# Kernel tuning notes

Measured on AMD Instinct MI355X. Metric: run time of the kernel, lower is better.

## Reference

```python
import jax, jax.numpy as jnp
import numpy as np

GRID_H, GRID_W, INPUT_DIM = 256, 256, 64
BATCH = 4096


def setup_inputs() -> dict:
    key = jax.random.key(0)
    k_in, k_w = jax.random.split(key)
    inputs = jax.random.uniform(k_in, (BATCH, INPUT_DIM), dtype=jnp.float32)
    # SOM weights initialized uniform[0,1) as in the original layer
    weights_map = jax.random.uniform(k_w, (GRID_H, GRID_W, INPUT_DIM), dtype=jnp.float32)
    return {"inputs": inputs, "weights_map": weights_map}


def reference(inputs, weights_map):
    """Inference forward of SOM2dLayer: find BMU coords + quantization error.

    inputs:      [B, D]
    weights_map: [H, W, D]
    returns (bmu_indices [B,2] int32, quantization_errors [B] float32)
    """
    H, W, D = weights_map.shape
    flat_w = weights_map.reshape(H * W, D)            # [N, D]
    x2 = jnp.sum(inputs * inputs, axis=1, keepdims=True)      # [B, 1]
    w2 = jnp.sum(flat_w * flat_w, axis=1)                     # [N]
    d2 = x2 - 2.0 * (inputs @ flat_w.T) + w2                  # [B, N]
    d2 = jnp.maximum(d2, 0.0)                                 # numerical floor
    bmu_flat = jnp.argmin(d2, axis=1)                         # [B]
    bmu_y = (bmu_flat // W).astype(jnp.int32)
    bmu_x = (bmu_flat % W).astype(jnp.int32)
    bmu_indices = jnp.stack([bmu_y, bmu_x], axis=1)           # [B, 2]
    min_d2 = jnp.take_along_axis(d2, bmu_flat[:, None], axis=1)[:, 0]
    quantization_errors = jnp.sqrt(min_d2)                    # [B]
    return bmu_indices, quantization_errors
```

## Files before the change

kernel.cpp:

```cpp
#include <hip/hip_runtime.h>
#include <math.h>


typedef short  bf16x8 __attribute__((ext_vector_type(8)));
typedef float  f32x4  __attribute__((ext_vector_type(4)));
typedef unsigned short u16;

constexpr int D     = 64;
constexpr int NW    = 65536;
constexpr int B     = 4096;
constexpr int NSUB  = 256;
constexpr int NFINE = NW / 16;
constexpr float MARG_HALF = 0.15f;

constexpr int NRANGE = 128;
constexpr int RBKB   = 8;

__device__ inline u16 bf16u(float f) {
    union { float f; unsigned u; } v; v.f = f;
    unsigned b = v.u;
    b += 0x7fffu + ((b >> 16) & 1u);
    return (u16)(b >> 16);
}

__device__ inline u16 bf16up(float f) {
    union { float f; unsigned u; } v; v.f = f;
    unsigned h = v.u >> 16;
    if ((v.u & 0xFFFFu) && !(v.u >> 31)) h += 1;
    return (u16)h;
}

__global__ __launch_bounds__(256) void k_prep(const float* __restrict__ w,
                                              const float* __restrict__ x,
                                              u16* __restrict__ whi,
                                              u16* __restrict__ xhi,
                                              float* __restrict__ w2c) {
    const int idx = blockIdx.x * 256 + threadIdx.x;
    if (idx < NW) {
        const float4* wr = reinterpret_cast<const float4*>(w + (size_t)idx * D);
        u16* orow = whi + (size_t)idx * D;
        float a0 = 0.f, a1 = 0.f, a2 = 0.f, a3 = 0.f;
#pragma unroll
        for (int h = 0; h < 8; ++h) {
            float4 v0 = wr[2 * h], v1 = wr[2 * h + 1];
            a0 = fmaf(v0.x, v0.x, a0); a1 = fmaf(v0.y, v0.y, a1);
            a2 = fmaf(v0.z, v0.z, a2); a3 = fmaf(v0.w, v0.w, a3);
            a0 = fmaf(v1.x, v1.x, a0); a1 = fmaf(v1.y, v1.y, a1);
            a2 = fmaf(v1.z, v1.z, a2); a3 = fmaf(v1.w, v1.w, a3);
            bf16x8 o = {(short)bf16u(v0.x), (short)bf16u(v0.y),
                        (short)bf16u(v0.z), (short)bf16u(v0.w),
                        (short)bf16u(v1.x), (short)bf16u(v1.y),
                        (short)bf16u(v1.z), (short)bf16u(v1.w)};
            *reinterpret_cast<bf16x8*>(orow + 8 * h) = o;
        }
        w2c[idx] = -0.5f * ((a0 + a1) + (a2 + a3));
    } else {
        const int r = idx - NW;
        const float4* xr = reinterpret_cast<const float4*>(x + (size_t)r * D);
        u16* orow = xhi + (size_t)r * D;
#pragma unroll
        for (int h = 0; h < 8; ++h) {
            float4 v0 = xr[2 * h], v1 = xr[2 * h + 1];
            bf16x8 o = {(short)bf16u(v0.x), (short)bf16u(v0.y),
                        (short)bf16u(v0.z), (short)bf16u(v0.w),
                        (short)bf16u(v1.x), (short)bf16u(v1.y),
                        (short)bf16u(v1.z), (short)bf16u(v1.w)};
            *reinterpret_cast<bf16x8*>(orow + 8 * h) = o;
        }
    }
}

template <int WRITE_FINE>
__global__ __launch_bounds__(256, 2) void k_screen0(
        const u16* __restrict__ whi, const u16* __restrict__ xhi,
        const float* __restrict__ w2c, float* __restrict__ pmt,
        u16* __restrict__ pmf) {
    __shared__ __align__(16) u16 fsh[4][2048];
    const int bid  = blockIdx.x;
    const int nr   = bid & (NRANGE - 1);
    const int tid  = threadIdx.x;
    const int wv   = tid >> 6;
    const int lane = tid & 63;
    const int col  = lane & 15;
    const int kg   = lane >> 4;
    const int rbk  = (bid >> 7) * 4 + wv;
    const int row0 = rbk * 128;
    const int W0   = nr * 512;

    bf16x8 a[8][2];
#pragma unroll
    for (int rg = 0; rg < 8; ++rg)
#pragma unroll
        for (int h = 0; h < 2; ++h)
            a[rg][h] = *reinterpret_cast<const bf16x8*>(
                xhi + (size_t)(row0 + rg * 16 + col) * D + h * 32 + kg * 8);

    float mx[8][4];
#pragma unroll
    for (int rg = 0; rg < 8; ++rg)
#pragma unroll
        for (int r = 0; r < 4; ++r) mx[rg][r] = -3.4e38f;

    bf16x8 pb[3][4];
    float  pc[3][2];

    const u16* wl = whi + (size_t)(W0 + col) * D + kg * 8;

    for (int ch = 0; ch < 2; ++ch) {
        const int pbase = ch * 8;
#pragma unroll
        for (int s = 0; s < 2; ++s) {
            const int pp = pbase + s;
            const u16* p0 = wl + (size_t)pp * 32 * D;
            const u16* p1 = p0 + 16 * D;
            pb[s][0] = *reinterpret_cast<const bf16x8*>(p0);
            pb[s][1] = *reinterpret_cast<const bf16x8*>(p0 + 32);
            pb[s][2] = *reinterpret_cast<const bf16x8*>(p1);
            pb[s][3] = *reinterpret_cast<const bf16x8*>(p1 + 32);
            pc[s][0] = w2c[W0 + pp * 32 + col];
            pc[s][1] = w2c[W0 + pp * 32 + 16 + col];
        }

#pragma unroll
        for (int mp = 0; mp < 8; ++mp) {
            if (mp + 2 < 8) {
                constexpr int dummy = 0; (void)dummy;
                const int sl = (mp + 2) % 3;
                const int pp = pbase + mp + 2;
                const u16* p0 = wl + (size_t)pp * 32 * D;
                const u16* p1 = p0 + 16 * D;
                pb[sl][0] = *reinterpret_cast<const bf16x8*>(p0);
                pb[sl][1] = *reinterpret_cast<const bf16x8*>(p0 + 32);
                pb[sl][2] = *reinterpret_cast<const bf16x8*>(p1);
                pb[sl][3] = *reinterpret_cast<const bf16x8*>(p1 + 32);
                pc[sl][0] = w2c[W0 + pp * 32 + col];
                pc[sl][1] = w2c[W0 + pp * 32 + 16 + col];
            }
            __builtin_amdgcn_sched_barrier(0);

            const int cs = mp % 3;
            const f32x4 cq0 = {pc[cs][0], pc[cs][0], pc[cs][0], pc[cs][0]};
            const f32x4 cq1 = {pc[cs][1], pc[cs][1], pc[cs][1], pc[cs][1]};
#pragma unroll
            for (int rg = 0; rg < 8; ++rg) {
                f32x4 acc = __builtin_amdgcn_mfma_f32_16x16x32_bf16(a[rg][0], pb[cs][0], cq0, 0, 0, 0);
                acc = __builtin_amdgcn_mfma_f32_16x16x32_bf16(a[rg][1], pb[cs][1], acc, 0, 0, 0);
                mx[rg][0] = fmaxf(mx[rg][0], acc[0]);
                mx[rg][1] = fmaxf(mx[rg][1], acc[1]);
                mx[rg][2] = fmaxf(mx[rg][2], acc[2]);
                mx[rg][3] = fmaxf(mx[rg][3], acc[3]);
            }
#pragma unroll
            for (int rg = 0; rg < 8; ++rg) {
                f32x4 acc = __builtin_amdgcn_mfma_f32_16x16x32_bf16(a[rg][0], pb[cs][2], cq1, 0, 0, 0);
                acc = __builtin_amdgcn_mfma_f32_16x16x32_bf16(a[rg][1], pb[cs][3], acc, 0, 0, 0);
                mx[rg][0] = fmaxf(mx[rg][0], acc[0]);
                mx[rg][1] = fmaxf(mx[rg][1], acc[1]);
                mx[rg][2] = fmaxf(mx[rg][2], acc[2]);
                mx[rg][3] = fmaxf(mx[rg][3], acc[3]);
            }
        }

        const int sub = nr * 2 + ch;

        if (WRITE_FINE) {
#pragma unroll
            for (int rg = 0; rg < 8; ++rg)
#pragma unroll
                for (int r = 0; r < 4; ++r)
                    fsh[wv][(rg * 16 + kg * 4 + r) * 16 + col] = bf16up(mx[rg][r]);
        }

#pragma unroll
        for (int rg = 0; rg < 8; ++rg) {
            float v0 = mx[rg][0], v1 = mx[rg][1], v2 = mx[rg][2], v3 = mx[rg][3];
#pragma unroll
            for (int sh = 1; sh < 16; sh <<= 1) {
                v0 = fmaxf(v0, __shfl_xor(v0, sh, 64));
                v1 = fmaxf(v1, __shfl_xor(v1, sh, 64));
                v2 = fmaxf(v2, __shfl_xor(v2, sh, 64));
                v3 = fmaxf(v3, __shfl_xor(v3, sh, 64));
            }
            float vv = v0;
            vv = (col == 1) ? v1 : vv;
            vv = (col == 2) ? v2 : vv;
            vv = (col == 3) ? v3 : vv;
            if (col < 4)
                pmt[(size_t)sub * B + row0 + rg * 16 + kg * 4 + col] = vv;
            mx[rg][0] = -3.4e38f; mx[rg][1] = -3.4e38f;
            mx[rg][2] = -3.4e38f; mx[rg][3] = -3.4e38f;
        }

        if (WRITE_FINE) {
            const char* src = reinterpret_cast<const char*>(&fsh[wv][0]);
            char* dst = (char*)pmf + ((size_t)sub * 32 + rbk) * 4096;
#pragma unroll
            for (int i = 0; i < 4; ++i)
                *reinterpret_cast<float4*>(dst + i * 1024 + lane * 16) =
                    *reinterpret_cast<const float4*>(src + i * 1024 + lane * 16);
        }
    }
}

template <int FINE>
__global__ __launch_bounds__(256) void k_rescore(
        const float* __restrict__ x, const float* __restrict__ w,
        const float* __restrict__ w2c, const float* __restrict__ pmt,
        const u16* __restrict__ pmf, float* __restrict__ out) {
    const int wv   = threadIdx.x >> 6;
    const int lane = threadIdx.x & 63;
    const int row  = blockIdx.x * 4 + wv;
    const int rbk2 = row >> 7;
    const int rl   = row & 127;

    float pv[4];
#pragma unroll
    for (int it = 0; it < 4; ++it)
        pv[it] = pmt[(size_t)(it * 64 + lane) * B + row];
    float gm = fmaxf(fmaxf(pv[0], pv[1]), fmaxf(pv[2], pv[3]));
#pragma unroll
    for (int s = 1; s < 64; s <<= 1) gm = fmaxf(gm, __shfl_xor(gm, s, 64));
    const float thr = gm - MARG_HALF;

    const float4* xr = reinterpret_cast<const float4*>(x + (size_t)row * D);
    float4 xq[16];
#pragma unroll
    for (int q = 0; q < 16; ++q) xq[q] = xr[q];

    float bestv = 3.4e38f;
    int   besti = 0x7fffffff;

#pragma unroll
    for (int it = 0; it < 4; ++it) {
        unsigned long long bm = __ballot(pv[it] >= thr);
        while (bm) {
            int sb = __ffsll(bm) - 1;
            bm &= bm - 1;
            int sub  = it * 64 + sb;
            int base = sub * 256;

            if (FINE) {
                float fv = -3.4e38f;
                if (lane < 16) {
                    union { unsigned u; float f; } c;
                    c.u = (unsigned)pmf[((size_t)sub * 32 + rbk2) * 2048
                                        + rl * 16 + lane] << 16;
                    fv = c.f;
                }
                unsigned long long fm = __ballot(fv >= thr);
                while (fm) {
                    int colq = __ffsll(fm) - 1;
                    fm &= fm - 1;
                    int j = lane & 15, q = lane >> 4;
                    int n = base + j * 16 + colq;
                    const float4* wr = reinterpret_cast<const float4*>(w + (size_t)n * D);
                    float d0 = 0.f, d1 = 0.f, d2 = 0.f, d3 = 0.f;
#pragma unroll
                    for (int k = 0; k < 4; ++k) {
                        float4 wq = wr[q * 4 + k];
                        float4 xv = xq[q * 4 + k];
                        d0 = fmaf(xv.x, wq.x, d0); d1 = fmaf(xv.y, wq.y, d1);
                        d2 = fmaf(xv.z, wq.z, d2); d3 = fmaf(xv.w, wq.w, d3);
                    }
                    float d = (d0 + d1) + (d2 + d3);
                    d += __shfl_xor(d, 16, 64);
                    d += __shfl_xor(d, 32, 64);
                    float val = -2.f * (d + w2c[n]);
                    if (val < bestv || (val == bestv && n < besti)) { bestv = val; besti = n; }
                }
            } else {
#pragma unroll
                for (int p4 = 0; p4 < 4; ++p4) {
                    int n = base + p4 * 64 + lane;
                    const float4* wr = reinterpret_cast<const float4*>(w + (size_t)n * D);
                    float d0 = 0.f, d1 = 0.f, d2 = 0.f, d3 = 0.f;
#pragma unroll
                    for (int q = 0; q < 16; ++q) {
                        float4 wq = wr[q];
                        d0 = fmaf(xq[q].x, wq.x, d0);
                        d1 = fmaf(xq[q].y, wq.y, d1);
                        d2 = fmaf(xq[q].z, wq.z, d2);
                        d3 = fmaf(xq[q].w, wq.w, d3);
                    }
                    float dot = (d0 + d1) + (d2 + d3);
                    float val = -2.f * (dot + w2c[n]);
                    if (val < bestv || (val == bestv && n < besti)) { bestv = val; besti = n; }
                }
            }
        }
    }
#pragma unroll
    for (int s = 1; s < 64; s <<= 1) {
        float ov = __shfl_xor(bestv, s, 64);
        int   oi = __shfl_xor(besti, s, 64);
        if (ov < bestv || (ov == bestv && oi < besti)) { bestv = ov; besti = oi; }
    }
    if (lane == 0) {
        float a0 = 0.f, a1 = 0.f, a2 = 0.f, a3 = 0.f;
#pragma unroll
        for (int q = 0; q < 16; ++q) {
            a0 = fmaf(xq[q].x, xq[q].x, a0);
            a1 = fmaf(xq[q].y, xq[q].y, a1);
            a2 = fmaf(xq[q].z, xq[q].z, a2);
            a3 = fmaf(xq[q].w, xq[q].w, a3);
        }
        float x2 = (a0 + a1) + (a2 + a3);
        float d2f = x2 + bestv;
        if (d2f < 0.f) d2f = 0.f;
        out[row * 2 + 0] = (float)(besti >> 8);
        out[row * 2 + 1] = (float)(besti & 255);
        out[2 * B + row] = sqrtf(d2f);
    }
}

__global__ __launch_bounds__(256) void fb_w2(const float* __restrict__ w,
                                             float* __restrict__ w2) {
    int n = blockIdx.x * 256 + threadIdx.x;
    const float4* wr = reinterpret_cast<const float4*>(w + (size_t)n * D);
    float a0 = 0.f, a1 = 0.f, a2 = 0.f, a3 = 0.f;
#pragma unroll
    for (int q = 0; q < 16; ++q) {
        float4 v = wr[q];
        a0 = fmaf(v.x, v.x, a0); a1 = fmaf(v.y, v.y, a1);
        a2 = fmaf(v.z, v.z, a2); a3 = fmaf(v.w, v.w, a3);
    }
    w2[n] = (a0 + a1) + (a2 + a3);
}

__global__ __launch_bounds__(256) void fb_main(const float* __restrict__ x,
                                               const float* __restrict__ w,
                                               const float* __restrict__ w2,
                                               float* __restrict__ ps,
                                               int* __restrict__ pi) {
    constexpr int NSTRIP = NW / 32;
    const int rb    = blockIdx.x & 15;
    const int strip = blockIdx.x >> 4;
    const int row   = rb * 256 + threadIdx.x;
    float xr[D];
    const float4* xrow = reinterpret_cast<const float4*>(x + (size_t)row * D);
#pragma unroll
    for (int q = 0; q < 16; ++q) {
        float4 v = xrow[q];
        xr[q * 4 + 0] = v.x; xr[q * 4 + 1] = v.y;
        xr[q * 4 + 2] = v.z; xr[q * 4 + 3] = v.w;
    }
    float best = 3.4e38f; int bidx = 0;
    const int n0 = strip * NSTRIP, n1 = n0 + NSTRIP;
    for (int n = n0; n < n1; ++n) {
        const float* wr = w + (size_t)n * D;
        float a0 = 0.f, a1 = 0.f, a2 = 0.f, a3 = 0.f;
#pragma unroll
        for (int d = 0; d < D; d += 4) {
            a0 = fmaf(xr[d + 0], wr[d + 0], a0);
            a1 = fmaf(xr[d + 1], wr[d + 1], a1);
            a2 = fmaf(xr[d + 2], wr[d + 2], a2);
            a3 = fmaf(xr[d + 3], wr[d + 3], a3);
        }
        float s = fmaf(-2.f, (a0 + a1) + (a2 + a3), w2[n]);
        if (s < best) { best = s; bidx = n; }
    }
    ps[(size_t)strip * B + row] = best;
    pi[(size_t)strip * B + row] = bidx;
}

__global__ __launch_bounds__(256) void fb_merge(const float* __restrict__ x,
                                                const float* __restrict__ ps,
                                                const int* __restrict__ pi,
                                                float* __restrict__ out) {
    int row = blockIdx.x * 256 + threadIdx.x;
    float bs = 3.5e38f; int bi = 0;
    for (int t = 0; t < 32; ++t) {
        float s = ps[(size_t)t * B + row];
        int   i = pi[(size_t)t * B + row];
        if (s < bs || (s == bs && i < bi)) { bs = s; bi = i; }
    }
    const float4* xrow = reinterpret_cast<const float4*>(x + (size_t)row * D);
    float a0 = 0.f, a1 = 0.f, a2 = 0.f, a3 = 0.f;
#pragma unroll
    for (int q = 0; q < 16; ++q) {
        float4 v = xrow[q];
        a0 = fmaf(v.x, v.x, a0); a1 = fmaf(v.y, v.y, a1);
        a2 = fmaf(v.z, v.z, a2); a3 = fmaf(v.w, v.w, a3);
    }
    float x2 = (a0 + a1) + (a2 + a3);
    float d2 = x2 + bs;
    if (d2 < 0.f) d2 = 0.f;
    out[row * 2 + 0] = (float)(bi >> 8);
    out[row * 2 + 1] = (float)(bi & 255);
    out[2 * B + row] = sqrtf(d2);
}

extern "C" void kernel_launch(void* const* d_in, const int* in_sizes, int n_in,
                              void* d_out, int out_size, void* d_ws, size_t ws_size,
                              hipStream_t stream) {
    const float* x = (const float*)d_in[0];
    const float* w = (const float*)d_in[1];
    float* out = (float*)d_out;

    const size_t whi_sz = (size_t)NW * D * 2;
    const size_t xhi_sz = (size_t)B * D * 2;
    const size_t w2c_sz = (size_t)NW * 4;
    const size_t pm_sz  = (size_t)B * NSUB * 4;
    const size_t pmf_sz = (size_t)NFINE * B * 2;
    const size_t need_c = whi_sz + xhi_sz + w2c_sz + pm_sz;
    const size_t need_f = need_c + pmf_sz;

    if (ws_size >= need_c) {
        char* p = (char*)d_ws;
        u16*   whi = (u16*)p;   p += whi_sz;
        u16*   xhi = (u16*)p;   p += xhi_sz;
        float* w2c = (float*)p; p += w2c_sz;
        float* pmt = (float*)p; p += pm_sz;
        u16*   pmf = (u16*)p;

        k_prep<<<(NW + B) / 256, 256, 0, stream>>>(w, x, whi, xhi, w2c);
        if (ws_size >= need_f) {
            k_screen0<1><<<NRANGE * RBKB, 256, 0, stream>>>(whi, xhi, w2c, pmt, pmf);
            k_rescore<1><<<B / 4, 256, 0, stream>>>(x, w, w2c, pmt, pmf, out);
        } else {
            k_screen0<0><<<NRANGE * RBKB, 256, 0, stream>>>(whi, xhi, w2c, pmt, pmf);
            k_rescore<0><<<B / 4, 256, 0, stream>>>(x, w, w2c, pmt, pmf, out);
        }
    } else {
        float* w2 = (float*)d_ws;
        float* ps = w2 + NW;
        int*   pi = (int*)(ps + (size_t)32 * B);
        fb_w2<<<NW / 256, 256, 0, stream>>>(w, w2);
        fb_main<<<16 * 32, 256, 0, stream>>>(x, w, w2, ps, pi);
        fb_merge<<<B / 256, 256, 0, stream>>>(x, ps, pi, out);
    }
}
```

Before: 115.9 us.

## Split prep rows across four threads and store per-row maxima row-major

The prep kernel now has four threads handle each 64-element row, using shuffles to reduce the squared norm. This gives more parallelism and better-coalesced loads than one thread per row. The per-subrange maxima buffer changes from subrange-major to row-major: screen writes two adjacent floats per row, and rescore reads each row's 256 maxima contiguously. A sched_barrier in the screen loop is also removed, which leaves instruction scheduling to the compiler.

```diff
diff --git a/kernel.cpp b/kernel.cpp
--- a/kernel.cpp
+++ b/kernel.cpp
@@ -4,6 +4,7 @@
 
 typedef short  bf16x8 __attribute__((ext_vector_type(8)));
 typedef float  f32x4  __attribute__((ext_vector_type(4)));
+typedef float  f32x2  __attribute__((ext_vector_type(2)));
 typedef unsigned short u16;
 
 constexpr int D     = 64;
@@ -35,13 +36,16 @@
                                               u16* __restrict__ whi,
                                               u16* __restrict__ xhi,
                                               float* __restrict__ w2c) {
-    const int idx = blockIdx.x * 256 + threadIdx.x;
-    if (idx < NW) {
-        const float4* wr = reinterpret_cast<const float4*>(w + (size_t)idx * D);
-        u16* orow = whi + (size_t)idx * D;
+    const int t = blockIdx.x * 256 + threadIdx.x;
+    if (t < 4 * NW) {
+        const int row = t >> 2;
+        const int q4  = t & 3;
+        const float4* wr = reinterpret_cast<const float4*>(
+            w + (size_t)row * D + q4 * 16);
+        u16* orow = whi + (size_t)row * D + q4 * 16;
         float a0 = 0.f, a1 = 0.f, a2 = 0.f, a3 = 0.f;
 #pragma unroll
-        for (int h = 0; h < 8; ++h) {
+        for (int h = 0; h < 2; ++h) {
             float4 v0 = wr[2 * h], v1 = wr[2 * h + 1];
             a0 = fmaf(v0.x, v0.x, a0); a1 = fmaf(v0.y, v0.y, a1);
             a2 = fmaf(v0.z, v0.z, a2); a3 = fmaf(v0.w, v0.w, a3);
@@ -53,13 +57,19 @@
                         (short)bf16u(v1.z), (short)bf16u(v1.w)};
             *reinterpret_cast<bf16x8*>(orow + 8 * h) = o;
         }
-        w2c[idx] = -0.5f * ((a0 + a1) + (a2 + a3));
+        float p = (a0 + a1) + (a2 + a3);
+        p += __shfl_xor(p, 1, 64);
+        p += __shfl_xor(p, 2, 64);
+        if (q4 == 0) w2c[row] = -0.5f * p;
     } else {
-        const int r = idx - NW;
-        const float4* xr = reinterpret_cast<const float4*>(x + (size_t)r * D);
-        u16* orow = xhi + (size_t)r * D;
-#pragma unroll
-        for (int h = 0; h < 8; ++h) {
+        const int t2  = t - 4 * NW;
+        const int row = t2 >> 2;
+        const int q4  = t2 & 3;
+        const float4* xr = reinterpret_cast<const float4*>(
+            x + (size_t)row * D + q4 * 16);
+        u16* orow = xhi + (size_t)row * D + q4 * 16;
+#pragma unroll
+        for (int h = 0; h < 2; ++h) {
             float4 v0 = xr[2 * h], v1 = xr[2 * h + 1];
             bf16x8 o = {(short)bf16u(v0.x), (short)bf16u(v0.y),
                         (short)bf16u(v0.z), (short)bf16u(v0.w),
@@ -73,7 +83,7 @@
 template <int WRITE_FINE>
 __global__ __launch_bounds__(256, 2) void k_screen0(
         const u16* __restrict__ whi, const u16* __restrict__ xhi,
-        const float* __restrict__ w2c, float* __restrict__ pmt,
+        const float* __restrict__ w2c, float* __restrict__ pm,
         u16* __restrict__ pmf) {
     __shared__ __align__(16) u16 fsh[4][2048];
     const int bid  = blockIdx.x;
@@ -101,9 +111,10 @@
 #pragma unroll
         for (int r = 0; r < 4; ++r) mx[rg][r] = -3.4e38f;
 
+    float pmk[8];
+
     bf16x8 pb[3][4];
     float  pc[3][2];
-
     const u16* wl = whi + (size_t)(W0 + col) * D + kg * 8;
 
     for (int ch = 0; ch < 2; ++ch) {
@@ -124,7 +135,6 @@
 #pragma unroll
         for (int mp = 0; mp < 8; ++mp) {
             if (mp + 2 < 8) {
-                constexpr int dummy = 0; (void)dummy;
                 const int sl = (mp + 2) % 3;
                 const int pp = pbase + mp + 2;
                 const u16* p0 = wl + (size_t)pp * 32 * D;
@@ -136,7 +146,6 @@
                 pc[sl][0] = w2c[W0 + pp * 32 + col];
                 pc[sl][1] = w2c[W0 + pp * 32 + 16 + col];
             }
-            __builtin_amdgcn_sched_barrier(0);
 
             const int cs = mp % 3;
             const f32x4 cq0 = {pc[cs][0], pc[cs][0], pc[cs][0], pc[cs][0]};
@@ -185,8 +194,13 @@
             vv = (col == 1) ? v1 : vv;
             vv = (col == 2) ? v2 : vv;
             vv = (col == 3) ? v3 : vv;
-            if (col < 4)
-                pmt[(size_t)sub * B + row0 + rg * 16 + kg * 4 + col] = vv;
+            if (ch == 0) {
+                pmk[rg] = vv;
+            } else if (col < 4) {
+                f32x2 pr = {pmk[rg], vv};
+                *reinterpret_cast<f32x2*>(
+                    &pm[(size_t)(row0 + rg * 16 + kg * 4 + col) * NSUB + nr * 2]) = pr;
+            }
             mx[rg][0] = -3.4e38f; mx[rg][1] = -3.4e38f;
             mx[rg][2] = -3.4e38f; mx[rg][3] = -3.4e38f;
         }
@@ -205,7 +219,7 @@
 template <int FINE>
 __global__ __launch_bounds__(256) void k_rescore(
         const float* __restrict__ x, const float* __restrict__ w,
-        const float* __restrict__ w2c, const float* __restrict__ pmt,
+        const float* __restrict__ w2c, const float* __restrict__ pm,
         const u16* __restrict__ pmf, float* __restrict__ out) {
     const int wv   = threadIdx.x >> 6;
     const int lane = threadIdx.x & 63;
@@ -216,7 +230,7 @@
     float pv[4];
 #pragma unroll
     for (int it = 0; it < 4; ++it)
-        pv[it] = pmt[(size_t)(it * 64 + lane) * B + row];
+        pv[it] = pm[(size_t)row * NSUB + it * 64 + lane];
     float gm = fmaxf(fmaxf(pv[0], pv[1]), fmaxf(pv[2], pv[3]));
 #pragma unroll
     for (int s = 1; s < 64; s <<= 1) gm = fmaxf(gm, __shfl_xor(gm, s, 64));
@@ -410,16 +424,16 @@
         u16*   whi = (u16*)p;   p += whi_sz;
         u16*   xhi = (u16*)p;   p += xhi_sz;
         float* w2c = (float*)p; p += w2c_sz;
-        float* pmt = (float*)p; p += pm_sz;
+        float* pm  = (float*)p; p += pm_sz;
         u16*   pmf = (u16*)p;
 
-        k_prep<<<(NW + B) / 256, 256, 0, stream>>>(w, x, whi, xhi, w2c);
+        k_prep<<<(4 * NW + 4 * B) / 256, 256, 0, stream>>>(w, x, whi, xhi, w2c);
         if (ws_size >= need_f) {
-            k_screen0<1><<<NRANGE * RBKB, 256, 0, stream>>>(whi, xhi, w2c, pmt, pmf);
-            k_rescore<1><<<B / 4, 256, 0, stream>>>(x, w, w2c, pmt, pmf, out);
+            k_screen0<1><<<NRANGE * RBKB, 256, 0, stream>>>(whi, xhi, w2c, pm, pmf);
+            k_rescore<1><<<B / 4, 256, 0, stream>>>(x, w, w2c, pm, pmf, out);
         } else {
-            k_screen0<0><<<NRANGE * RBKB, 256, 0, stream>>>(whi, xhi, w2c, pmt, pmf);
-            k_rescore<0><<<B / 4, 256, 0, stream>>>(x, w, w2c, pmt, pmf, out);
+            k_screen0<0><<<NRANGE * RBKB, 256, 0, stream>>>(whi, xhi, w2c, pm, pmf);
+            k_rescore<0><<<B / 4, 256, 0, stream>>>(x, w, w2c, pm, pmf, out);
         }
     } else {
         float* w2 = (float*)d_ws;
```

After: 137.6 us. 18.8% more time.
